# Optimization experiments

Measured on AMD Instinct MI355X. Metric: run time of the kernel, lower is better.

## Reference

```python
import jax, jax.numpy as jnp
import numpy as np

DIM = 1024
NUM_HEADS = 16
HEAD_DIM = DIM // NUM_HEADS
BINDING_BIAS = 0.5
SCALE = HEAD_DIM ** -0.5


def setup_inputs() -> dict:
    key = jax.random.key(0)
    ks = jax.random.split(key, 10)
    B, S, D = 2, 2048, DIM
    std = D ** -0.5
    return {
        "x": jax.random.normal(ks[0], (B, S, D), jnp.float32),
        "binding_matrix": jax.random.uniform(ks[1], (S, S), jnp.float32),
        "Wq": jax.random.normal(ks[2], (D, D), jnp.float32) * std,
        "bq": jnp.zeros((D,), jnp.float32),
        "Wk": jax.random.normal(ks[3], (D, D), jnp.float32) * std,
        "bk": jnp.zeros((D,), jnp.float32),
        "Wv": jax.random.normal(ks[4], (D, D), jnp.float32) * std,
        "bv": jnp.zeros((D,), jnp.float32),
        "Wo": jax.random.normal(ks[5], (D, D), jnp.float32) * std,
        "bo": jnp.zeros((D,), jnp.float32),
    }


def reference(x, binding_matrix, Wq, bq, Wk, bk, Wv, bv, Wo, bo):
    B, S, D = x.shape
    H, Hd = NUM_HEADS, HEAD_DIM
    # projections -> [B, H, S, Hd]
    q = (x @ Wq + bq).reshape(B, S, H, Hd).transpose(0, 2, 1, 3)
    k = (x @ Wk + bk).reshape(B, S, H, Hd).transpose(0, 2, 1, 3)
    v = (x @ Wv + bv).reshape(B, S, H, Hd).transpose(0, 2, 1, 3)
    # scores [B, H, S, S] with additive binding bias
    attn = jnp.einsum("bhqd,bhkd->bhqk", q, k) * SCALE
    attn = attn + BINDING_BIAS * binding_matrix[None, None, :, :]
    attn = jax.nn.softmax(attn, axis=-1)
    out = jnp.einsum("bhqk,bhkd->bhqd", attn, v)
    out = out.transpose(0, 2, 1, 3).reshape(B, S, D)
    return out @ Wo + bo
```

## Files before the change

### kernel.cpp

```cpp
#include <hip/hip_runtime.h>

#define DEV static __device__ __forceinline__

typedef __attribute__((ext_vector_type(4))) float f32x4;
typedef __attribute__((ext_vector_type(8))) __bf16 bfv8;
typedef __attribute__((ext_vector_type(8))) short s8v;
typedef __attribute__((ext_vector_type(4))) short s4v;

DEV short f2bf(float f) {
    unsigned u = __float_as_uint(f);
    u = (u + 0x7fffu + ((u >> 16) & 1u)) >> 16;
    return (short)u;
}
DEV float bf2f(short s) { return __uint_as_float(((unsigned)(unsigned short)s) << 16); }

DEV void gload16(const void* g, void* l) {
    __builtin_amdgcn_global_load_lds(
        (const __attribute__((address_space(1))) void*)g,
        (__attribute__((address_space(3))) void*)l, 16, 0, 0);
}

DEV f32x4 mfma16(bfv8 a, bfv8 b, f32x4 c) {
    return __builtin_amdgcn_mfma_f32_16x16x32_bf16(a, b, c, 0, 0, 0);
}

DEV float max3f(float a, float b, float c) {
    float d;
    asm("v_max3_f32 %0, %1, %2, %3" : "=v"(d) : "v"(a), "v"(b), "v"(c));
    return d;
}
DEV unsigned cvtpk(float lo, float hi) {
    unsigned w;
    asm("v_cvt_pk_bf16_f32 %0, %1, %2" : "=v"(w) : "v"(lo), "v"(hi));
    return w;
}

DEV bfv8 ldsfrag(const short* base, int row, int slog) {
    int sp = slog ^ (row & 7);
    return *reinterpret_cast<const bfv8*>(base + row * 64 + sp * 8);
}

__global__ void k_cvt(const float* __restrict__ in, short* __restrict__ out, float s) {
    int i = blockIdx.x * blockDim.x + threadIdx.x;
    const float4* p = (const float4*)in + (size_t)i * 2;
    float4 a = p[0], b = p[1];
    s8v o;
    o[0] = f2bf(a.x * s); o[1] = f2bf(a.y * s); o[2] = f2bf(a.z * s); o[3] = f2bf(a.w * s);
    o[4] = f2bf(b.x * s); o[5] = f2bf(b.y * s); o[6] = f2bf(b.z * s); o[7] = f2bf(b.w * s);
    reinterpret_cast<s8v*>(out)[i] = o;
}

__global__ void k_transpose4(
    const float* __restrict__ W0, const float* __restrict__ W1,
    const float* __restrict__ W2, const float* __restrict__ W3,
    short* __restrict__ T0, short* __restrict__ T1,
    short* __restrict__ T2, short* __restrict__ T3, float s0)
{
    __shared__ float tl[32][33];
    const int z = blockIdx.z;
    const float* W = z == 0 ? W0 : z == 1 ? W1 : z == 2 ? W2 : W3;
    short* Wt = z == 0 ? T0 : z == 1 ? T1 : z == 2 ? T2 : T3;
    const float s = z == 0 ? s0 : 1.f;
    int tx = threadIdx.x & 31, ty = threadIdx.x >> 5;
    int nb = blockIdx.x * 32, kb = blockIdx.y * 32;
#pragma unroll
    for (int i = 0; i < 4; i++)
        tl[ty + i * 8][tx] = W[(kb + ty + i * 8) * 1024 + nb + tx];
    __syncthreads();
#pragma unroll
    for (int i = 0; i < 4; i++)
        Wt[(nb + ty + i * 8) * 1024 + kb + tx] = f2bf(tl[tx][ty + i * 8] * s);
}

template <int EPI>
DEV void gemm_body(const short* __restrict__ A, const short* __restrict__ Bt,
                   const float* __restrict__ bias, void* __restrict__ outp,
                   float bscale, int row0, int col0, short* As, short* Bs)
{
    const int t = threadIdx.x, lane = t & 63;
    const int wv = t >> 6, wr = wv >> 1, wc = wv & 1;
    const int g = lane >> 4, c = lane & 15;

    const f32x4 z4 = {0.f, 0.f, 0.f, 0.f};
    f32x4 acc[2][4];
#pragma unroll
    for (int m = 0; m < 2; m++)
#pragma unroll
        for (int n = 0; n < 4; n++) acc[m][n] = z4;

    for (int kt = 0; kt < 16; ++kt) {
        const int k0 = kt * 64;
        const short* Ag = A + row0 * 1024 + k0;
        const short* Bg = Bt + col0 * 1024 + k0;
#pragma unroll
        for (int j = 0; j < 2; j++) {
            int idx = j * 256 + t;
            int row = idx >> 3, sp = idx & 7, sl = sp ^ (row & 7);
            gload16(Ag + row * 1024 + sl * 8, As + idx * 8);
        }
#pragma unroll
        for (int j = 0; j < 4; j++) {
            int idx = j * 256 + t;
            int row = idx >> 3, sp = idx & 7, sl = sp ^ (row & 7);
            gload16(Bg + row * 1024 + sl * 8, Bs + idx * 8);
        }
        __syncthreads();

        bfv8 af[2][2], bfr[4][2];
#pragma unroll
        for (int m = 0; m < 2; m++)
#pragma unroll
            for (int ks = 0; ks < 2; ks++)
                af[m][ks] = ldsfrag(As, wr * 32 + m * 16 + c, ks * 4 + g);
#pragma unroll
        for (int n = 0; n < 4; n++)
#pragma unroll
            for (int ks = 0; ks < 2; ks++)
                bfr[n][ks] = ldsfrag(Bs, wc * 64 + n * 16 + c, ks * 4 + g);
        __builtin_amdgcn_s_setprio(1);
#pragma unroll
        for (int m = 0; m < 2; m++)
#pragma unroll
            for (int n = 0; n < 4; n++)
#pragma unroll
                for (int ks = 0; ks < 2; ks++)
                    acc[m][n] = mfma16(af[m][ks], bfr[n][ks], acc[m][n]);
        __builtin_amdgcn_s_setprio(0);
        __syncthreads();
    }

#pragma unroll
    for (int n = 0; n < 4; n++) {
        const int gc = col0 + wc * 64 + n * 16 + c;
        const float bvl = bias[gc] * bscale;
        const int h = gc >> 6, d = gc & 63;
#pragma unroll
        for (int m = 0; m < 2; m++) {
            const int gr = row0 + wr * 32 + m * 16 + g * 4;
            if (EPI == 2) {
                float* O = (float*)outp;
#pragma unroll
                for (int r = 0; r < 4; r++) O[(gr + r) * 1024 + gc] = acc[m][n][r] + bvl;
            } else {
                const int b = gr >> 11, sr = gr & 2047;
                short* O = (short*)outp;
                if (EPI == 0) {
                    int base = ((b * 16 + h) * 2048 + sr) * 64 + d;
#pragma unroll
                    for (int r = 0; r < 4; r++) O[base + r * 64] = f2bf(acc[m][n][r] + bvl);
                } else {
                    s4v vv;
#pragma unroll
                    for (int r = 0; r < 4; r++) vv[r] = f2bf(acc[m][n][r] + bvl);
                    *reinterpret_cast<s4v*>(O + ((b * 16 + h) * 64 + d) * 2048 + sr) = vv;
                }
            }
        }
    }
}

__global__ __launch_bounds__(256, 2) void k_gemm3(
    const short* __restrict__ A,
    const short* __restrict__ WqT, const short* __restrict__ WkT, const short* __restrict__ WvT,
    const float* __restrict__ bq, const float* __restrict__ bk, const float* __restrict__ bv,
    short* __restrict__ Qs, short* __restrict__ Kst, short* __restrict__ Vts, float scq)
{
    __shared__ alignas(16) short As[64 * 64];
    __shared__ alignas(16) short Bs[128 * 64];
    const int which = blockIdx.y >> 3;
    const int col0 = (blockIdx.y & 7) * 128;
    const int row0 = blockIdx.x * 64;
    if (which == 0)
        gemm_body<0>(A, WqT, bq, Qs, scq, row0, col0, As, Bs);
    else if (which == 1)
        gemm_body<0>(A, WkT, bk, Kst, 1.f, row0, col0, As, Bs);
    else
        gemm_body<1>(A, WvT, bv, Vts, 1.f, row0, col0, As, Bs);
}

__global__ __launch_bounds__(256, 2) void k_gemmO(
    const short* __restrict__ A, const short* __restrict__ Bt,
    const float* __restrict__ bias, float* __restrict__ outp)
{
    __shared__ alignas(16) short As[64 * 64];
    __shared__ alignas(16) short Bs[128 * 64];
    gemm_body<2>(A, Bt, bias, outp, 1.f, blockIdx.x * 64, blockIdx.y * 128, As, Bs);
}

__global__ __launch_bounds__(256, 4) void k_attn(
    const short* __restrict__ Q, const short* __restrict__ K,
    const short* __restrict__ Vt, const short* __restrict__ bb,
    short* __restrict__ Ob)
{
    __shared__ alignas(16) short Ks[2][64 * 64];
    __shared__ alignas(16) short Vs[2][64 * 64];
    __shared__ alignas(16) short Ps[4][16 * 64];
    const int t = threadIdx.x, lane = t & 63;
    const int wv = t >> 6, g = lane >> 4, c = lane & 15;
    const int qt = blockIdx.x, bh = blockIdx.y;
    const int b = bh >> 4, h = bh & 15;
    const short* Qb = Q + bh * 2048 * 64;
    const short* Kb = K + bh * 2048 * 64;
    const short* Vb = Vt + bh * 64 * 2048;
    const int q0 = qt * 64 + wv * 16;

    bfv8 qf[2];
#pragma unroll
    for (int ks = 0; ks < 2; ks++)
        qf[ks] = *reinterpret_cast<const bfv8*>(Qb + (q0 + c) * 64 + ks * 32 + g * 8);

    const f32x4 z4 = {0.f, 0.f, 0.f, 0.f};
    f32x4 oa[4];
#pragma unroll
    for (int nd = 0; nd < 4; nd++) oa[nd] = z4;
    f32x4 lacc = z4;
    float mrun = 20.0f;

    s8v ob_;
#pragma unroll
    for (int i = 0; i < 8; i++) ob_[i] = (short)0x3F80;
    const bfv8 ones = __builtin_bit_cast(bfv8, ob_);

    const int idx0 = t, idx1 = 256 + t;
    const int r0 = idx0 >> 3, s0 = ((idx0 & 7) ^ (r0 & 7)) * 8;
    const int r1 = idx1 >> 3, s1 = ((idx1 & 7) ^ (r1 & 7)) * 8;
    const short* kp0 = Kb + r0 * 64 + s0;
    const short* kp1 = Kb + r1 * 64 + s1;
    const short* vp0 = Vb + r0 * 2048 + s0;
    const short* vp1 = Vb + r1 * 2048 + s1;
    const short* bbp = bb + (size_t)(q0 + c) * 2048 + 4 * g;

    char* Pb = (char*)&Ps[wv][0];
    const int rx = c & 7;
    char* pw[4];
#pragma unroll
    for (int n = 0; n < 4; n++)
        pw[n] = Pb + c * 128 + (((2 * n + (g >> 1)) ^ rx) << 4) + ((g & 1) << 3);
    const char* pr0 = Pb + c * 128 + ((g ^ rx) << 4);
    const char* pr1 = Pb + c * 128 + (((4 + g) ^ rx) << 4);

    gload16(kp0, &Ks[0][idx0 * 8]);
    gload16(kp1, &Ks[0][idx1 * 8]);
    gload16(vp0, &Vs[0][idx0 * 8]);
    gload16(vp1, &Vs[0][idx1 * 8]);
    kp0 += 4096; kp1 += 4096; vp0 += 64; vp1 += 64;
    s4v bn[4];
#pragma unroll
    for (int n = 0; n < 4; n++) bn[n] = *reinterpret_cast<const s4v*>(bbp + n * 16);
    bbp += 64;
    __syncthreads();

    for (int kt = 0; kt < 32; ++kt) {
        const int cur = kt & 1;
        f32x4 cb[4];
#pragma unroll
        for (int n = 0; n < 4; n++)
#pragma unroll
            for (int r = 0; r < 4; r++) cb[n][r] = bf2f(bn[n][r]);
        if (kt < 31) {
            const int nb = cur ^ 1;
            gload16(kp0, &Ks[nb][idx0 * 8]);
            gload16(kp1, &Ks[nb][idx1 * 8]);
            gload16(vp0, &Vs[nb][idx0 * 8]);
            gload16(vp1, &Vs[nb][idx1 * 8]);
            kp0 += 4096; kp1 += 4096; vp0 += 64; vp1 += 64;
#pragma unroll
            for (int n = 0; n < 4; n++) bn[n] = *reinterpret_cast<const s4v*>(bbp + n * 16);
            bbp += 64;
        }

        const short* Kc = &Ks[cur][0];
        const short* Vc = &Vs[cur][0];

        f32x4 sc[4];
        __builtin_amdgcn_s_setprio(1);
#pragma unroll
        for (int n = 0; n < 4; n++) {
            bfv8 k0 = ldsfrag(Kc, n * 16 + c, g);
            bfv8 k1 = ldsfrag(Kc, n * 16 + c, 4 + g);
            sc[n] = mfma16(k0, qf[0], cb[n]);
            sc[n] = mfma16(k1, qf[1], sc[n]);
        }
        __builtin_amdgcn_s_setprio(0);

#pragma unroll
        for (int n = 0; n < 4; n++)
#pragma unroll
            for (int r = 0; r < 4; r++)
                sc[n][r] = __builtin_amdgcn_exp2f(sc[n][r] - mrun);

#pragma unroll
        for (int n = 0; n < 4; n++) {
            uint2 wp;
            wp.x = cvtpk(sc[n][0], sc[n][1]);
            wp.y = cvtpk(sc[n][2], sc[n][3]);
            *reinterpret_cast<uint2*>(pw[n]) = wp;
        }

        bfv8 pa0 = *reinterpret_cast<const bfv8*>(pr0);
        bfv8 pa1 = *reinterpret_cast<const bfv8*>(pr1);
        __builtin_amdgcn_s_setprio(1);
#pragma unroll
        for (int nd = 0; nd < 4; nd++) {
            bfv8 v0 = ldsfrag(Vc, nd * 16 + c, g);
            bfv8 v1 = ldsfrag(Vc, nd * 16 + c, 4 + g);
            oa[nd] = mfma16(v0, pa0, oa[nd]);
            oa[nd] = mfma16(v1, pa1, oa[nd]);
        }
        lacc = mfma16(ones, pa0, lacc);
        lacc = mfma16(ones, pa1, lacc);
        __builtin_amdgcn_s_setprio(0);

        float t0 = fmaxf(max3f(sc[0][0], sc[0][1], sc[0][2]), sc[0][3]);
        float t1 = fmaxf(max3f(sc[1][0], sc[1][1], sc[1][2]), sc[1][3]);
        float t2 = fmaxf(max3f(sc[2][0], sc[2][1], sc[2][2]), sc[2][3]);
        float t3 = fmaxf(max3f(sc[3][0], sc[3][1], sc[3][2]), sc[3][3]);
        float pemax = fmaxf(max3f(t0, t1, t2), t3);
        if (!__all(pemax <= 2896.0f)) {
            float rmax = fmaxf(pemax, __shfl_xor(pemax, 16));
            rmax = fmaxf(rmax, __shfl_xor(rmax, 32));
            if (rmax > 2896.0f) {
                const float corr = 1.0f / rmax;
                mrun += __log2f(rmax);
#pragma unroll
                for (int nd = 0; nd < 4; nd++)
#pragma unroll
                    for (int r = 0; r < 4; r++) oa[nd][r] *= corr;
#pragma unroll
                for (int r = 0; r < 4; r++) lacc[r] *= corr;
            }
        }
        __syncthreads();
    }

    const float rl = 1.0f / lacc[0];
    const size_t srow = (size_t)(b * 2048 + q0 + c);
#pragma unroll
    for (int nd = 0; nd < 4; nd++) {
        s4v st;
#pragma unroll
        for (int r = 0; r < 4; r++) st[r] = f2bf(oa[nd][r] * rl);
        *reinterpret_cast<s4v*>(Ob + srow * 1024 + h * 64 + nd * 16 + 4 * g) = st;
    }
}

extern "C" void kernel_launch(void* const* d_in, const int* in_sizes, int n_in,
                              void* d_out, int out_size, void* d_ws, size_t ws_size,
                              hipStream_t stream)
{
    (void)in_sizes; (void)n_in; (void)out_size; (void)ws_size;
    const float* x    = (const float*)d_in[0];
    const float* bind = (const float*)d_in[1];
    const float* Wq   = (const float*)d_in[2];
    const float* bq   = (const float*)d_in[3];
    const float* Wk   = (const float*)d_in[4];
    const float* bk   = (const float*)d_in[5];
    const float* Wv   = (const float*)d_in[6];
    const float* bv   = (const float*)d_in[7];
    const float* Wo   = (const float*)d_in[8];
    const float* bo   = (const float*)d_in[9];

    char* ws = (char*)d_ws;
    const size_t MB = (size_t)1 << 20;
    short* xb   = (short*)(ws + 0 * MB);
    short* Wqt  = (short*)(ws + 8 * MB);
    short* Wkt  = (short*)(ws + 10 * MB);
    short* Wvt  = (short*)(ws + 12 * MB);
    short* Wot  = (short*)(ws + 14 * MB);
    short* bbm  = (short*)(ws + 16 * MB);
    short* Qs   = (short*)(ws + 24 * MB);
    short* Kst  = (short*)(ws + 32 * MB);
    short* Vts  = (short*)(ws + 40 * MB);
    short* Obuf = (short*)(ws + 48 * MB);

    const float LOG2E = 1.4426950408889634f;
    const float SCQ = 0.125f * LOG2E;
    const float SCB = 0.5f * LOG2E;

    k_cvt<<<2048, 256, 0, stream>>>(x, xb, 1.f);
    k_cvt<<<2048, 256, 0, stream>>>(bind, bbm, SCB);
    k_transpose4<<<dim3(32, 32, 4), 256, 0, stream>>>(Wq, Wk, Wv, Wo,
                                                      Wqt, Wkt, Wvt, Wot, SCQ);
    k_gemm3<<<dim3(64, 24), 256, 0, stream>>>(xb, Wqt, Wkt, Wvt, bq, bk, bv,
                                              Qs, Kst, Vts, SCQ);
    k_attn<<<dim3(32, 32), 256, 0, stream>>>(Qs, Kst, Vts, bbm, Obuf);
    k_gemmO<<<dim3(64, 8), 256, 0, stream>>>(Obuf, Wot, bo, (float*)d_out);
}
```

Baseline: 151.2 us.

## Keep P in registers by permuting V fragment loads instead of LDS round-trip

Result: slower. 192.7 us (+27.4%).

```diff
diff --git a/kernel.cpp b/kernel.cpp
--- a/kernel.cpp
+++ b/kernel.cpp
@@ -33,6 +33,12 @@
     unsigned w;
     asm("v_cvt_pk_bf16_f32 %0, %1, %2" : "=v"(w) : "v"(lo), "v"(hi));
     return w;
+}
+
+typedef struct { s4v lo, hi; } s4x2;
+DEV bfv8 combine64(s4v a, s4v b) {
+    s4x2 p; p.lo = a; p.hi = b;
+    return __builtin_bit_cast(bfv8, p);
 }
 
 DEV bfv8 ldsfrag(const short* base, int row, int slog) {
@@ -187,14 +193,13 @@
     gemm_body<2>(A, Bt, bias, outp, 1.f, blockIdx.x * 64, blockIdx.y * 128, As, Bs);
 }
 
-__global__ __launch_bounds__(256, 4) void k_attn(
+__global__ __launch_bounds__(256, 5) void k_attn(
     const short* __restrict__ Q, const short* __restrict__ K,
     const short* __restrict__ Vt, const short* __restrict__ bb,
     short* __restrict__ Ob)
 {
     __shared__ alignas(16) short Ks[2][64 * 64];
     __shared__ alignas(16) short Vs[2][64 * 64];
-    __shared__ alignas(16) short Ps[4][16 * 64];
     const int t = threadIdx.x, lane = t & 63;
     const int wv = t >> 6, g = lane >> 4, c = lane & 15;
     const int qt = blockIdx.x, bh = blockIdx.y;
@@ -230,14 +235,13 @@
     const short* vp1 = Vb + r1 * 2048 + s1;
     const short* bbp = bb + (size_t)(q0 + c) * 2048 + 4 * g;
 
-    char* Pb = (char*)&Ps[wv][0];
-    const int rx = c & 7;
-    char* pw[4];
-#pragma unroll
-    for (int n = 0; n < 4; n++)
-        pw[n] = Pb + c * 128 + (((2 * n + (g >> 1)) ^ rx) << 4) + ((g & 1) << 3);
-    const char* pr0 = Pb + c * 128 + ((g ^ rx) << 4);
-    const char* pr1 = Pb + c * 128 + (((4 + g) ^ rx) << 4);
+    const int cx = c & 7;
+    const int kofs0 = c * 128 + ((g ^ cx) << 4);
+    const int kofs1 = c * 128 + (((4 + g) ^ cx) << 4);
+    int vof[4];
+#pragma unroll
+    for (int m = 0; m < 4; m++)
+        vof[m] = c * 128 + ((((2 * m) + (g >> 1)) ^ cx) << 4) + ((g & 1) << 3);
 
     gload16(kp0, &Ks[0][idx0 * 8]);
     gload16(kp1, &Ks[0][idx1 * 8]);
@@ -269,15 +273,15 @@
             bbp += 64;
         }
 
-        const short* Kc = &Ks[cur][0];
-        const short* Vc = &Vs[cur][0];
+        const char* Kc = (const char*)&Ks[cur][0];
+        const char* Vc = (const char*)&Vs[cur][0];
 
         f32x4 sc[4];
         __builtin_amdgcn_s_setprio(1);
 #pragma unroll
         for (int n = 0; n < 4; n++) {
-            bfv8 k0 = ldsfrag(Kc, n * 16 + c, g);
-            bfv8 k1 = ldsfrag(Kc, n * 16 + c, 4 + g);
+            bfv8 k0 = *reinterpret_cast<const bfv8*>(Kc + kofs0 + n * 2048);
+            bfv8 k1 = *reinterpret_cast<const bfv8*>(Kc + kofs1 + n * 2048);
             sc[n] = mfma16(k0, qf[0], cb[n]);
             sc[n] = mfma16(k1, qf[1], sc[n]);
         }
@@ -289,26 +293,31 @@
             for (int r = 0; r < 4; r++)
                 sc[n][r] = __builtin_amdgcn_exp2f(sc[n][r] - mrun);
 
+        unsigned w0[4], w1[4];
 #pragma unroll
         for (int n = 0; n < 4; n++) {
-            uint2 wp;
-            wp.x = cvtpk(sc[n][0], sc[n][1]);
-            wp.y = cvtpk(sc[n][2], sc[n][3]);
-            *reinterpret_cast<uint2*>(pw[n]) = wp;
-        }
-
-        bfv8 pa0 = *reinterpret_cast<const bfv8*>(pr0);
-        bfv8 pa1 = *reinterpret_cast<const bfv8*>(pr1);
+            w0[n] = cvtpk(sc[n][0], sc[n][1]);
+            w1[n] = cvtpk(sc[n][2], sc[n][3]);
+        }
+        s4v pw0; pw0[0] = (short)(w0[0] & 0xffff);
+        typedef struct { unsigned a, b, c2, d; } u4;
+        u4 q0w; q0w.a = w0[0]; q0w.b = w1[0]; q0w.c2 = w0[1]; q0w.d = w1[1];
+        u4 q1w; q1w.a = w0[2]; q1w.b = w1[2]; q1w.c2 = w0[3]; q1w.d = w1[3];
+        bfv8 pf0 = __builtin_bit_cast(bfv8, q0w);
+        bfv8 pf1 = __builtin_bit_cast(bfv8, q1w);
+
         __builtin_amdgcn_s_setprio(1);
 #pragma unroll
         for (int nd = 0; nd < 4; nd++) {
-            bfv8 v0 = ldsfrag(Vc, nd * 16 + c, g);
-            bfv8 v1 = ldsfrag(Vc, nd * 16 + c, 4 + g);
-            oa[nd] = mfma16(v0, pa0, oa[nd]);
-            oa[nd] = mfma16(v1, pa1, oa[nd]);
-        }
-        lacc = mfma16(ones, pa0, lacc);
-        lacc = mfma16(ones, pa1, lacc);
+            s4v a00 = *reinterpret_cast<const s4v*>(Vc + vof[0] + nd * 2048);
+            s4v a01 = *reinterpret_cast<const s4v*>(Vc + vof[1] + nd * 2048);
+            s4v a10 = *reinterpret_cast<const s4v*>(Vc + vof[2] + nd * 2048);
+            s4v a11 = *reinterpret_cast<const s4v*>(Vc + vof[3] + nd * 2048);
+            oa[nd] = mfma16(combine64(a00, a01), pf0, oa[nd]);
+            oa[nd] = mfma16(combine64(a10, a11), pf1, oa[nd]);
+        }
+        lacc = mfma16(ones, pf0, lacc);
+        lacc = mfma16(ones, pf1, lacc);
         __builtin_amdgcn_s_setprio(0);
 
         float t0 = fmaxf(max3f(sc[0][0], sc[0][1], sc[0][2]), sc[0][3]);
```
